# Kernel tuning notes

Hardware: AMD Instinct MI355X
Metric: run time of the kernel (lower is better)

## Reference

```python
import jax, jax.numpy as jnp
import numpy as np

B, N, DIM = 2, 2048, 1024
HEADS, DH = 16, 64
INNER = HEADS * DH
LN_EPS = 1e-5


def setup_inputs() -> dict:
    key = jax.random.key(0)
    ks = jax.random.split(key, 3)
    x = jax.random.normal(ks[0], (B, N, DIM), dtype=jnp.float32)
    ln_w = jnp.ones((DIM,), dtype=jnp.float32)
    ln_b = jnp.zeros((DIM,), dtype=jnp.float32)
    w_qkv = jax.random.normal(ks[1], (DIM, 3 * INNER), dtype=jnp.float32) * (DIM ** -0.5)
    w_out = jax.random.normal(ks[2], (INNER, DIM), dtype=jnp.float32) * (INNER ** -0.5)
    b_out = jnp.zeros((DIM,), dtype=jnp.float32)
    return {"x": x, "ln_w": ln_w, "ln_b": ln_b, "w_qkv": w_qkv, "w_out": w_out, "b_out": b_out}


def _rope(q, k):
    # q, k: (b, h, n, d) with d even; interleaved RoPE matching the torch module.
    n, d = q.shape[-2], q.shape[-1]
    inv_freq = jnp.exp(jnp.arange(0, d, 2, dtype=jnp.float32) * (-jnp.log(jnp.float32(10000.0)) / d))
    ang = jnp.arange(n, dtype=jnp.float32)[:, None] * inv_freq[None, :]  # (n, d/2)
    cos = jnp.repeat(jnp.cos(ang), 2, axis=-1)  # (n, d) -> broadcast over b,h
    sin = jnp.repeat(jnp.sin(ang), 2, axis=-1)

    def rot(t):
        t2 = t.reshape(*t.shape[:-1], d // 2, 2)  # pairs (even, odd)
        t2 = jnp.stack([-t2[..., 1], t2[..., 0]], axis=-1).reshape(t.shape)
        return t * cos + t2 * sin

    return rot(q), rot(k)


def reference(x, ln_w, ln_b, w_qkv, w_out, b_out):
    # LayerNorm
    mu = jnp.mean(x, axis=-1, keepdims=True)
    var = jnp.var(x, axis=-1, keepdims=True)
    xn = (x - mu) * jax.lax.rsqrt(var + LN_EPS) * ln_w + ln_b
    # QKV projection (no bias)
    qkv = xn @ w_qkv  # (b, n, 3*inner)
    q, k, v = jnp.split(qkv, 3, axis=-1)
    split_heads = lambda t: t.reshape(B, N, HEADS, DH).transpose(0, 2, 1, 3)  # b h n d
    q, k, v = split_heads(q), split_heads(k), split_heads(v)
    q, k = _rope(q, k)
    scale = DH ** -0.5
    dots = jnp.einsum('bhid,bhjd->bhij', q, k) * scale
    attn = jax.nn.softmax(dots, axis=-1)
    out = jnp.einsum('bhij,bhjd->bhid', attn, v)
    out = out.transpose(0, 2, 1, 3).reshape(B, N, INNER)  # b n (h d)
    return out @ w_out + b_out
```

## Files before the change

kernel.cpp:

```cpp
#include <hip/hip_runtime.h>

typedef unsigned short u16;
typedef unsigned int   u32;
typedef __bf16 bf16x8 __attribute__((ext_vector_type(8)));
typedef __bf16 bf16x2 __attribute__((ext_vector_type(2)));
typedef float  f32x4  __attribute__((ext_vector_type(4)));

#define B_     2
#define N_     2048
#define DIM_   1024
#define HEADS_ 16
#define DH_    64
#define BH_    (B_*HEADS_)
#define ROWS_  (B_*N_)

__device__ __forceinline__ u16 f2b(float f) {
  union { __bf16 h; u16 u; } v; v.h = (__bf16)f; return v.u;
}
__device__ __forceinline__ u32 pkb(float a, float b) {
  bf16x2 t; t[0] = (__bf16)a; t[1] = (__bf16)b;
  union { bf16x2 v; u32 u; } c; c.v = t; return c.u;
}
__device__ __forceinline__ float b2f(u16 h) {
  union { u32 u; float f; } v; v.u = ((u32)h) << 16;
  return v.f;
}
__device__ __forceinline__ void gload16(const void* g, void* l) {
  __builtin_amdgcn_global_load_lds(
      (const __attribute__((address_space(1))) void*)g,
      (__attribute__((address_space(3))) void*)l, 16, 0, 0);
}
__device__ __forceinline__ f32x4 mfma16(bf16x8 a, bf16x8 b, f32x4 c) {
  return __builtin_amdgcn_mfma_f32_16x16x32_bf16(a, b, c, 0, 0, 0);
}

__global__ __launch_bounds__(256) void ln_kernel(const float* __restrict__ x,
    const float* __restrict__ lw, const float* __restrict__ lb,
    u16* __restrict__ xn) {
  int r = blockIdx.x, t = threadIdx.x;
  const float4* xr = (const float4*)(x + (size_t)r * DIM_);
  float4 v = xr[t];
  float s  = v.x + v.y + v.z + v.w;
  float s2 = v.x*v.x + v.y*v.y + v.z*v.z + v.w*v.w;
  #pragma unroll
  for (int off = 32; off >= 1; off >>= 1) {
    s  += __shfl_down(s, off);
    s2 += __shfl_down(s2, off);
  }
  __shared__ float ps[4], ps2[4], bc[2];
  int w = t >> 6, lane = t & 63;
  if (lane == 0) { ps[w] = s; ps2[w] = s2; }
  __syncthreads();
  if (t == 0) {
    float S = ps[0]+ps[1]+ps[2]+ps[3], S2 = ps2[0]+ps2[1]+ps2[2]+ps2[3];
    float mu = S * (1.0f/DIM_);
    float var = S2 * (1.0f/DIM_) - mu*mu;
    bc[0] = mu; bc[1] = rsqrtf(var + 1e-5f);
  }
  __syncthreads();
  float mu = bc[0], rs = bc[1];
  float4 wv = ((const float4*)lw)[t];
  float4 bv = ((const float4*)lb)[t];
  u32 lo = pkb((v.x-mu)*rs*wv.x + bv.x, (v.y-mu)*rs*wv.y + bv.y);
  u32 hi = pkb((v.z-mu)*rs*wv.z + bv.z, (v.w-mu)*rs*wv.w + bv.w);
  ((uint2*)xn)[(size_t)r*256 + t] = make_uint2(lo, hi);
}

__global__ __launch_bounds__(256) void transpose_f32_bf16(const float* __restrict__ in,
    u16* __restrict__ out, int R, int C) {
  __shared__ float tile[32][33];
  int tx = threadIdx.x & 31, ty = threadIdx.x >> 5;
  int c0 = blockIdx.x * 32, r0 = blockIdx.y * 32;
  #pragma unroll
  for (int i = 0; i < 4; i++)
    tile[ty + i*8][tx] = in[(size_t)(r0 + ty + i*8) * C + c0 + tx];
  __syncthreads();
  #pragma unroll
  for (int i = 0; i < 4; i++)
    out[(size_t)(c0 + ty + i*8) * R + r0 + tx] = f2b(tile[tx][ty + i*8]);
}

template<int MODE>
__global__ __launch_bounds__(256) void gemm_bt(
    const u16* __restrict__ A, const u16* __restrict__ Bt, int N, int K,
    u16* __restrict__ qo, u16* __restrict__ ko, u16* __restrict__ vo,
    const float* __restrict__ bias, float* __restrict__ out) {
  __shared__ __align__(16) u16 lA[128*32];
  __shared__ __align__(16) u16 lB[128*32];
  int tid = threadIdx.x;
  int lane = tid & 63;
  int w = tid >> 6, wm = w >> 1, wn = w & 1;
  int l15 = lane & 15, g = lane >> 4;
  int bm = blockIdx.x, bn = blockIdx.y;
  const f32x4 z = {0.f, 0.f, 0.f, 0.f};
  f32x4 acc[4][4];
  #pragma unroll
  for (int i = 0; i < 4; i++)
    #pragma unroll
    for (int j = 0; j < 4; j++)
      acc[i][j] = z;
  const u16* ag = A  + (size_t)(bm*128 + (tid>>2)) * K + (tid&3)*8;
  const u16* bg = Bt + (size_t)(bn*128 + (tid>>2)) * K + (tid&3)*8;
  u16* la = lA + tid*8;
  u16* lb = lB + tid*8;
  for (int k0 = 0; k0 < K; k0 += 32) {
    gload16(ag + k0,                la);
    gload16(ag + (size_t)64*K + k0, la + 2048);
    gload16(bg + k0,                lb);
    gload16(bg + (size_t)64*K + k0, lb + 2048);
    __syncthreads();
    bf16x8 af[4], bfr[4];
    #pragma unroll
    for (int mt = 0; mt < 4; mt++)
      af[mt] = *(const bf16x8*)(lA + (wm*64 + mt*16 + l15)*32 + g*8);
    #pragma unroll
    for (int nt = 0; nt < 4; nt++)
      bfr[nt] = *(const bf16x8*)(lB + (wn*64 + nt*16 + l15)*32 + g*8);
    __builtin_amdgcn_s_setprio(1);
    #pragma unroll
    for (int mt = 0; mt < 4; mt++)
      #pragma unroll
      for (int nt = 0; nt < 4; nt++)
        acc[mt][nt] = mfma16(af[mt], bfr[nt], acc[mt][nt]);
    __builtin_amdgcn_s_setprio(0);
    __syncthreads();
  }
  #pragma unroll
  for (int mt = 0; mt < 4; mt++) {
    #pragma unroll
    for (int nt = 0; nt < 4; nt++) {
      #pragma unroll
      for (int reg = 0; reg < 4; reg++) {
        int rr = bm*128 + wm*64 + mt*16 + g*4 + reg;
        int cc = bn*128 + wn*64 + nt*16 + l15;
        float val = acc[mt][nt][reg];
        if (MODE == 0) {
          int which = cc >> 10, inner = cc & 1023;
          int h = inner >> 6, dd = inner & 63;
          int b = rr >> 11, np = rr & 2047;
          int bh = b*HEADS_ + h;
          if (which == 0)      qo[((size_t)(bh*2048 + np))*64 + dd] = f2b(val);
          else if (which == 1) ko[((size_t)(bh*2048 + np))*64 + dd] = f2b(val);
          else                 vo[((size_t)(bh*64 + dd))*2048 + np] = f2b(val);
        } else {
          out[(size_t)rr * N + cc] = val + bias[cc];
        }
      }
    }
  }
}

__global__ __launch_bounds__(256) void rope_kernel(u16* q, u16* k) {
  int tid = blockIdx.x * 256 + threadIdx.x;
  int row = tid >> 3, sub = tid & 7;
  int n = row & 2047;
  u32* qp = (u32*)(q + (size_t)row * 64 + sub * 8);
  u32* kp = (u32*)(k + (size_t)row * 64 + sub * 8);
  uint4 uq = *(uint4*)qp;
  uint4 uk = *(uint4*)kp;
  float c4[4], s4[4];
  #pragma unroll
  for (int j = 0; j < 4; j++) {
    int p = sub*4 + j;
    float freq = expf(-(2.0f * (float)p) * (9.210340371976184f / 64.0f));
    float ang = (float)n * freq;
    __sincosf(ang, &s4[j], &c4[j]);
  }
  const float qs = 0.125f * 1.4426950408889634f;
#define ROPE_Q(u, c, s) { \
    float e = b2f((u16)(u)), o = b2f((u16)((u) >> 16)); \
    (u) = pkb((e*(c) - o*(s))*qs, (o*(c) + e*(s))*qs); }
#define ROPE_K(u, c, s) { \
    float e = b2f((u16)(u)), o = b2f((u16)((u) >> 16)); \
    (u) = pkb(e*(c) - o*(s), o*(c) + e*(s)); }
  ROPE_Q(uq.x, c4[0], s4[0]) ROPE_Q(uq.y, c4[1], s4[1])
  ROPE_Q(uq.z, c4[2], s4[2]) ROPE_Q(uq.w, c4[3], s4[3])
  ROPE_K(uk.x, c4[0], s4[0]) ROPE_K(uk.y, c4[1], s4[1])
  ROPE_K(uk.z, c4[2], s4[2]) ROPE_K(uk.w, c4[3], s4[3])
#undef ROPE_Q
#undef ROPE_K
  *(uint4*)qp = uq;
  *(uint4*)kp = uk;
}

__global__ __launch_bounds__(512, 4) void flash_attn(
    const u16* __restrict__ qbf, const u16* __restrict__ kbf,
    const u16* __restrict__ vt, u16* __restrict__ aout) {
  __shared__ __align__(16) char smem[49152];
  char* lK = smem;
  char* lV = smem + 24576;
  int tid = threadIdx.x;
  int w = tid >> 6, lane = tid & 63;
  int l15 = lane & 15, g = lane >> 4;
  int p = w & 3, rho = w >> 2;
  int lin = blockIdx.x;
  int nb = (lin & 7) * 64 + (lin >> 3);
  int bh = nb >> 4, qb = nb & 15;
  const f32x4 z = {0.f, 0.f, 0.f, 0.f};
  const u16* qrow_base = qbf + ((size_t)bh*2048 + qb*128 + p*32) * 64;
  bf16x8 Qf[2][2];
  #pragma unroll
  for (int qt = 0; qt < 2; qt++)
    #pragma unroll
    for (int dh = 0; dh < 2; dh++)
      Qf[qt][dh] = *(const bf16x8*)(qrow_base + (qt*16 + l15)*64 + dh*32 + g*8);
  const char* kb = (const char*)(kbf + (size_t)bh * 2048 * 64);
  const char* vb = (const char*)(vt  + (size_t)bh * 64 * 2048);
  int srow = tid >> 3;
  int soff = ((tid & 7) * 16) ^ ((srow & 7) << 4);
  int sl = srow & 31;
  int ksrc = (srow & 32) | (((sl >> 2) & 3) << 3) | (((sl >> 4) & 1) << 2) | (sl & 3);
  const int swz = (l15 & 7) << 4;

  float lp[2][2] = {{0.f, 0.f}, {0.f, 0.f}};
  f32x4 o[4][2];
  #pragma unroll
  for (int i = 0; i < 4; i++)
    #pragma unroll
    for (int j = 0; j < 2; j++)
      o[i][j] = z;

#define STAGE(t, buf) { \
    gload16(kb + (size_t)((t)*64 + ksrc) * 128 + soff, lK + (buf)*8192 + (size_t)tid*16); \
    gload16(vb + (size_t)srow * 4096 + (t)*128 + soff, lV + (buf)*8192 + (size_t)tid*16); }

  STAGE(0, 0)
  STAGE(1, 1)
  asm volatile("s_waitcnt vmcnt(2)" ::: "memory");
  __builtin_amdgcn_s_barrier();

  int cur = 0, pfb = 2;
  #pragma unroll 1
  for (int t = 0; t < 32; ++t) {
    if (t < 30) STAGE(t + 2, pfb)
    const char* Kc = lK + cur*8192;
    const char* Vc = lV + cur*8192;
    f32x4 st[2][2];
    bf16x8 ka[2][2];
    #pragma unroll
    for (int kt = 0; kt < 2; kt++)
      #pragma unroll
      for (int dh = 0; dh < 2; dh++)
        ka[kt][dh] = *(const bf16x8*)(Kc + (rho*32 + kt*16 + l15)*128
                                         + ((dh*64 + g*16) ^ swz));
    __builtin_amdgcn_s_setprio(1);
    #pragma unroll
    for (int kt = 0; kt < 2; kt++)
      #pragma unroll
      for (int qt = 0; qt < 2; qt++) {
        f32x4 a = mfma16(ka[kt][0], Qf[qt][0], z);
        st[kt][qt] = mfma16(ka[kt][1], Qf[qt][1], a);
      }
    __builtin_amdgcn_s_setprio(0);
    #pragma unroll
    for (int kt = 0; kt < 2; kt++)
      #pragma unroll
      for (int qt = 0; qt < 2; qt++)
        #pragma unroll
        for (int r = 0; r < 4; r++) {
          float pv = __builtin_amdgcn_exp2f(st[kt][qt][r]);
          st[kt][qt][r] = pv;
          lp[qt][kt] += pv;
        }
    bf16x8 vf[4];
    #pragma unroll
    for (int dt = 0; dt < 4; dt++)
      vf[dt] = *(const bf16x8*)(Vc + (dt*16 + l15)*128 + ((rho*64 + g*16) ^ swz));
    __builtin_amdgcn_s_setprio(1);
    #pragma unroll
    for (int qt = 0; qt < 2; qt++) {
      union { u32 u[4]; bf16x8 v; } pf;
      pf.u[0] = pkb(st[0][qt][0], st[0][qt][1]);
      pf.u[1] = pkb(st[0][qt][2], st[0][qt][3]);
      pf.u[2] = pkb(st[1][qt][0], st[1][qt][1]);
      pf.u[3] = pkb(st[1][qt][2], st[1][qt][3]);
      #pragma unroll
      for (int dt = 0; dt < 4; dt++)
        o[dt][qt] = mfma16(vf[dt], pf.v, o[dt][qt]);
    }
    __builtin_amdgcn_s_setprio(0);
    if (t < 31) {
      if (t < 30) { asm volatile("s_waitcnt vmcnt(2)" ::: "memory"); }
      else        { asm volatile("s_waitcnt vmcnt(0)" ::: "memory"); }
      __builtin_amdgcn_s_barrier();
    }
    cur = (cur + 1 == 3) ? 0 : cur + 1;
    pfb = (pfb + 1 == 3) ? 0 : pfb + 1;
  }
#undef STAGE

  float ls[2];
  #pragma unroll
  for (int qt = 0; qt < 2; qt++) {
    ls[qt] = lp[qt][0] + lp[qt][1];
    ls[qt] += __shfl_xor(ls[qt], 16);
    ls[qt] += __shfl_xor(ls[qt], 32);
  }
  __syncthreads();

  float* lspx = (float*)(smem + 32768);
  if (rho == 1) {
    #pragma unroll
    for (int dt = 0; dt < 4; dt++)
      #pragma unroll
      for (int qt = 0; qt < 2; qt++) {
        int ql = qt*16 + l15;
        int off = p*8192 + ql*256 + ((dt*64 + g*16) ^ ((ql & 7) << 4));
        *(f32x4*)(smem + off) = o[dt][qt];
      }
    if (g == 0) {
      lspx[p*64 + l15]      = ls[0];
      lspx[p*64 + 16 + l15] = ls[1];
    }
  }
  __syncthreads();
  float rls[2] = {0.f, 0.f};
  if (rho == 0) {
    #pragma unroll
    for (int qt = 0; qt < 2; qt++)
      rls[qt] = 1.0f / (ls[qt] + lspx[p*64 + qt*16 + l15]);
    #pragma unroll
    for (int dt = 0; dt < 4; dt++)
      #pragma unroll
      for (int qt = 0; qt < 2; qt++) {
        int ql = qt*16 + l15;
        int off = p*8192 + ql*256 + ((dt*64 + g*16) ^ ((ql & 7) << 4));
        o[dt][qt] += *(const f32x4*)(smem + off);
      }
  }
  __syncthreads();
  if (rho == 0) {
    #pragma unroll
    for (int dt = 0; dt < 4; dt++)
      #pragma unroll
      for (int qt = 0; qt < 2; qt++) {
        int ql = qt*16 + l15;
        u32 w0 = pkb(o[dt][qt][0]*rls[qt], o[dt][qt][1]*rls[qt]);
        u32 w1 = pkb(o[dt][qt][2]*rls[qt], o[dt][qt][3]*rls[qt]);
        int d2 = dt*32 + g*8;
        *(uint2*)(smem + p*8192 + ql*128 + (d2 ^ ((ql & 7) << 4))) =
            make_uint2(w0, w1);
      }
  }
  __syncthreads();
  int row = tid >> 2;
  int b = bh >> 4, h = bh & 15;
  int n = qb*128 + row;
  #pragma unroll
  for (int j = 0; j < 2; j++) {
    int slot = (tid & 3)*2 + j;
    uint4 rv = *(const uint4*)(smem + (row >> 5)*8192 + (row & 31)*128
                               + ((slot*16) ^ ((row & 7) << 4)));
    *(uint4*)(aout + ((size_t)(b*2048 + n))*1024 + h*64 + slot*8) = rv;
  }
}

extern "C" void kernel_launch(void* const* d_in, const int* in_sizes, int n_in,
                              void* d_out, int out_size, void* d_ws, size_t ws_size,
                              hipStream_t stream) {
  const float* x    = (const float*)d_in[0];
  const float* lw   = (const float*)d_in[1];
  const float* lb   = (const float*)d_in[2];
  const float* wqkv = (const float*)d_in[3];
  const float* wout = (const float*)d_in[4];
  const float* bout = (const float*)d_in[5];
  float* out = (float*)d_out;

  char* ws = (char*)d_ws;
  size_t off = 0;
  auto alloc = [&](size_t bytes) {
    char* p = ws + off;
    off += (bytes + 255) & ~(size_t)255;
    return p;
  };
  u16* xn   = (u16*)alloc((size_t)ROWS_*DIM_*2);
  u16* wqt  = (u16*)alloc((size_t)3072*1024*2);
  u16* wot  = (u16*)alloc((size_t)1024*1024*2);
  u16* qb   = (u16*)alloc((size_t)BH_*2048*64*2);
  u16* kb   = (u16*)alloc((size_t)BH_*2048*64*2);
  u16* vtb  = (u16*)alloc((size_t)BH_*2048*64*2);
  u16* aout = (u16*)alloc((size_t)ROWS_*1024*2);

  ln_kernel<<<ROWS_, 256, 0, stream>>>(x, lw, lb, xn);
  transpose_f32_bf16<<<dim3(96, 32), 256, 0, stream>>>(wqkv, wqt, 1024, 3072);
  transpose_f32_bf16<<<dim3(32, 32), 256, 0, stream>>>(wout, wot, 1024, 1024);
  gemm_bt<0><<<dim3(32, 24), 256, 0, stream>>>(xn, wqt, 3072, 1024,
                                               qb, kb, vtb, nullptr, nullptr);
  rope_kernel<<<2048, 256, 0, stream>>>(qb, kb);
  flash_attn<<<512, 512, 0, stream>>>(qb, kb, vtb, aout);
  gemm_bt<1><<<dim3(32, 8), 256, 0, stream>>>(aout, wot, 1024, 1024,
                                              nullptr, nullptr, nullptr, bout, out);
}
```

Measured before the change: 124.5 us.

## Replace QKV GEMM with 256x256-tile double-buffered kernel using swizzled LDS

Adds a dedicated QKV projection GEMM with 256x256 output tiles, 512 threads, BK=64, double-buffered direct global-to-LDS loads with an XOR swizzle, and interleaved LDS reads and MFMA issue under raised wave priority. Blocks are remapped so that consecutive blocks share B tiles, for better L2 reuse. The larger tile is meant to raise arithmetic intensity and overlap loads with compute. The costs are 128KB of LDS per block, heavy register pressure from a 32-tile accumulator, and only 192 blocks on a 256-CU device, which leaves some CUs idle.

```diff
diff --git a/kernel.cpp b/kernel.cpp
--- a/kernel.cpp
+++ b/kernel.cpp
@@ -78,6 +78,102 @@
   #pragma unroll
   for (int i = 0; i < 4; i++)
     out[(size_t)(c0 + ty + i*8) * R + r0 + tx] = f2b(tile[tx][ty + i*8]);
+}
+
+__global__ __launch_bounds__(512, 2) void gemm256_qkv(
+    const u16* __restrict__ A, const u16* __restrict__ Bt,
+    u16* __restrict__ qo, u16* __restrict__ ko, u16* __restrict__ vo) {
+  __shared__ __align__(16) char lds[131072];
+  const int K = 1024;
+  int tid = threadIdx.x;
+  int lane = tid & 63;
+  int w = tid >> 6, wm = w >> 2, wn = w & 3;
+  int l15 = lane & 15, g = lane >> 4;
+  int lin = blockIdx.x;
+  int nb = (lin & 7) * 24 + (lin >> 3);
+  int bm = nb & 15, bn = nb >> 4;
+  int srow = tid >> 3;
+  int ssoff = ((tid & 7) * 16) ^ ((srow & 7) << 4);
+  const char* Ab = (const char*)A;
+  const char* Bb = (const char*)Bt;
+  const int swz = (l15 & 7) << 4;
+
+  f32x4 acc[8][4];
+  #pragma unroll
+  for (int i = 0; i < 8; i++)
+    #pragma unroll
+    for (int j = 0; j < 4; j++)
+      acc[i][j] = (f32x4){0.f, 0.f, 0.f, 0.f};
+
+#define SA(t, buf) { _Pragma("unroll") for (int j = 0; j < 4; j++) \
+    gload16(Ab + ((size_t)(bm*256 + j*64 + srow) * K + (size_t)(t)*64) * 2 + ssoff, \
+            lds + (buf)*65536 + j*8192 + tid*16); }
+#define SB(t, buf) { _Pragma("unroll") for (int j = 0; j < 4; j++) \
+    gload16(Bb + ((size_t)(bn*256 + j*64 + srow) * K + (size_t)(t)*64) * 2 + ssoff, \
+            lds + (buf)*65536 + 32768 + j*8192 + tid*16); }
+#define RDA(qm) { _Pragma("unroll") for (int mt = 0; mt < 4; mt++) { \
+    const char* ar = lA + (wm*128 + ((qm)*4 + mt)*16 + l15)*128; \
+    af[mt][0] = *(const bf16x8*)(ar + ((g*16) ^ swz)); \
+    af[mt][1] = *(const bf16x8*)(ar + ((64 + g*16) ^ swz)); } }
+#define RDB(qn) { _Pragma("unroll") for (int nt = 0; nt < 2; nt++) { \
+    const char* br = lB + (wn*64 + ((qn)*2 + nt)*16 + l15)*128; \
+    bfr[nt][0] = *(const bf16x8*)(br + ((g*16) ^ swz)); \
+    bfr[nt][1] = *(const bf16x8*)(br + ((64 + g*16) ^ swz)); } }
+#define MM(qm, qn) { __builtin_amdgcn_s_setprio(1); \
+    _Pragma("unroll") for (int mt = 0; mt < 4; mt++) \
+    _Pragma("unroll") for (int nt = 0; nt < 2; nt++) { \
+      f32x4 c = acc[(qm)*4 + mt][(qn)*2 + nt]; \
+      c = mfma16(af[mt][0], bfr[nt][0], c); \
+      c = mfma16(af[mt][1], bfr[nt][1], c); \
+      acc[(qm)*4 + mt][(qn)*2 + nt] = c; } \
+    __builtin_amdgcn_s_setprio(0); }
+
+  SA(0, 0) SB(0, 0) SA(1, 1) SB(1, 1)
+  __syncthreads();
+
+  #pragma unroll 1
+  for (int t = 0; t < 16; ++t) {
+    const char* lA = lds + (t & 1)*65536;
+    const char* lB = lA + 32768;
+    int nbuf = (t + 1) & 1;
+    bf16x8 af[4][2], bfr[2][2];
+    RDA(0) RDB(0)
+    if (t >= 1 && t < 15) SA(t + 1, nbuf)
+    MM(0, 0)
+    RDB(1)
+    if (t >= 1 && t < 15) SB(t + 1, nbuf)
+    MM(0, 1)
+    RDA(1) RDB(0)
+    MM(1, 0)
+    RDB(1)
+    MM(1, 1)
+    if (t < 15) __syncthreads();
+  }
+#undef SA
+#undef SB
+#undef RDA
+#undef RDB
+#undef MM
+
+  #pragma unroll
+  for (int mi = 0; mi < 8; mi++) {
+    #pragma unroll
+    for (int ni = 0; ni < 4; ni++) {
+      #pragma unroll
+      for (int reg = 0; reg < 4; reg++) {
+        int rr = bm*256 + wm*128 + mi*16 + g*4 + reg;
+        int cc = bn*256 + wn*64 + ni*16 + l15;
+        float val = acc[mi][ni][reg];
+        int which = cc >> 10, inner = cc & 1023;
+        int h = inner >> 6, dd = inner & 63;
+        int b = rr >> 11, np = rr & 2047;
+        int bh = b*HEADS_ + h;
+        if (which == 0)      qo[((size_t)(bh*2048 + np))*64 + dd] = f2b(val);
+        else if (which == 1) ko[((size_t)(bh*2048 + np))*64 + dd] = f2b(val);
+        else                 vo[((size_t)(bh*64 + dd))*2048 + np] = f2b(val);
+      }
+    }
+  }
 }
 
 template<int MODE>
@@ -384,8 +480,7 @@
   ln_kernel<<<ROWS_, 256, 0, stream>>>(x, lw, lb, xn);
   transpose_f32_bf16<<<dim3(96, 32), 256, 0, stream>>>(wqkv, wqt, 1024, 3072);
   transpose_f32_bf16<<<dim3(32, 32), 256, 0, stream>>>(wout, wot, 1024, 1024);
-  gemm_bt<0><<<dim3(32, 24), 256, 0, stream>>>(xn, wqt, 3072, 1024,
-                                               qb, kb, vtb, nullptr, nullptr);
+  gemm256_qkv<<<192, 512, 0, stream>>>(xn, wqt, qb, kb, vtb);
   rope_kernel<<<2048, 256, 0, stream>>>(qb, kb);
   flash_attn<<<512, 512, 0, stream>>>(qb, kb, vtb, aout);
   gemm_bt<1><<<dim3(32, 8), 256, 0, stream>>>(aout, wot, 1024, 1024,
```

Result: slower. 140.1 us (+12.5%).

## Fuse prep kernels, fold RoPE into QKV GEMM epilogue, retile output GEMM

Applied to the files above, without the earlier changes.

Merges layernorm, both weight transposes and a cos/sin table build into one prep launch. RoPE and the query scale are applied inside the QKV GEMM epilogue, with the partner element fetched by lane shuffle, which removes the separate RoPE read/write pass over Q and K. The output projection GEMM becomes a dedicated kernel with 128x64 tiles, doubling the block count for better CU occupancy. The trade-offs are extra cos/sin table loads per epilogue element and more total B-tile traffic in the output GEMM.

```diff
diff --git a/kernel.cpp b/kernel.cpp
--- a/kernel.cpp
+++ b/kernel.cpp
@@ -34,57 +34,76 @@
   return __builtin_amdgcn_mfma_f32_16x16x32_bf16(a, b, c, 0, 0, 0);
 }
 
-__global__ __launch_bounds__(256) void ln_kernel(const float* __restrict__ x,
-    const float* __restrict__ lw, const float* __restrict__ lb,
-    u16* __restrict__ xn) {
-  int r = blockIdx.x, t = threadIdx.x;
-  const float4* xr = (const float4*)(x + (size_t)r * DIM_);
-  float4 v = xr[t];
-  float s  = v.x + v.y + v.z + v.w;
-  float s2 = v.x*v.x + v.y*v.y + v.z*v.z + v.w*v.w;
-  #pragma unroll
-  for (int off = 32; off >= 1; off >>= 1) {
-    s  += __shfl_down(s, off);
-    s2 += __shfl_down(s2, off);
-  }
-  __shared__ float ps[4], ps2[4], bc[2];
-  int w = t >> 6, lane = t & 63;
-  if (lane == 0) { ps[w] = s; ps2[w] = s2; }
-  __syncthreads();
-  if (t == 0) {
-    float S = ps[0]+ps[1]+ps[2]+ps[3], S2 = ps2[0]+ps2[1]+ps2[2]+ps2[3];
-    float mu = S * (1.0f/DIM_);
-    float var = S2 * (1.0f/DIM_) - mu*mu;
-    bc[0] = mu; bc[1] = rsqrtf(var + 1e-5f);
-  }
-  __syncthreads();
-  float mu = bc[0], rs = bc[1];
-  float4 wv = ((const float4*)lw)[t];
-  float4 bv = ((const float4*)lb)[t];
-  u32 lo = pkb((v.x-mu)*rs*wv.x + bv.x, (v.y-mu)*rs*wv.y + bv.y);
-  u32 hi = pkb((v.z-mu)*rs*wv.z + bv.z, (v.w-mu)*rs*wv.w + bv.w);
-  ((uint2*)xn)[(size_t)r*256 + t] = make_uint2(lo, hi);
-}
-
-__global__ __launch_bounds__(256) void transpose_f32_bf16(const float* __restrict__ in,
-    u16* __restrict__ out, int R, int C) {
+__global__ __launch_bounds__(256) void prep_kernel(
+    const float* __restrict__ x, const float* __restrict__ lw,
+    const float* __restrict__ lb, const float* __restrict__ wqkv,
+    const float* __restrict__ wout, u16* __restrict__ xn,
+    u16* __restrict__ wqt, u16* __restrict__ wot,
+    float* __restrict__ cosT, float* __restrict__ sinT) {
   __shared__ float tile[32][33];
-  int tx = threadIdx.x & 31, ty = threadIdx.x >> 5;
-  int c0 = blockIdx.x * 32, r0 = blockIdx.y * 32;
-  #pragma unroll
-  for (int i = 0; i < 4; i++)
-    tile[ty + i*8][tx] = in[(size_t)(r0 + ty + i*8) * C + c0 + tx];
-  __syncthreads();
-  #pragma unroll
-  for (int i = 0; i < 4; i++)
-    out[(size_t)(c0 + ty + i*8) * R + r0 + tx] = f2b(tile[tx][ty + i*8]);
-}
-
-template<int MODE>
-__global__ __launch_bounds__(256) void gemm_bt(
-    const u16* __restrict__ A, const u16* __restrict__ Bt, int N, int K,
-    u16* __restrict__ qo, u16* __restrict__ ko, u16* __restrict__ vo,
-    const float* __restrict__ bias, float* __restrict__ out) {
+  int blk = blockIdx.x, t = threadIdx.x;
+  if (blk < 4096) {
+    int r = blk;
+    const float4* xr = (const float4*)(x + (size_t)r * DIM_);
+    float4 v = xr[t];
+    float s  = v.x + v.y + v.z + v.w;
+    float s2 = v.x*v.x + v.y*v.y + v.z*v.z + v.w*v.w;
+    #pragma unroll
+    for (int off = 32; off >= 1; off >>= 1) {
+      s  += __shfl_down(s, off);
+      s2 += __shfl_down(s2, off);
+    }
+    int w = t >> 6, lane = t & 63;
+    if (lane == 0) { tile[0][w] = s; tile[1][w] = s2; }
+    __syncthreads();
+    if (t == 0) {
+      float S = tile[0][0]+tile[0][1]+tile[0][2]+tile[0][3];
+      float S2 = tile[1][0]+tile[1][1]+tile[1][2]+tile[1][3];
+      float mu = S * (1.0f/DIM_);
+      float var = S2 * (1.0f/DIM_) - mu*mu;
+      tile[2][0] = mu; tile[2][1] = rsqrtf(var + 1e-5f);
+    }
+    __syncthreads();
+    float mu = tile[2][0], rs = tile[2][1];
+    float4 wv = ((const float4*)lw)[t];
+    float4 bv = ((const float4*)lb)[t];
+    u32 lo = pkb((v.x-mu)*rs*wv.x + bv.x, (v.y-mu)*rs*wv.y + bv.y);
+    u32 hi = pkb((v.z-mu)*rs*wv.z + bv.z, (v.w-mu)*rs*wv.w + bv.w);
+    ((uint2*)xn)[(size_t)r*256 + t] = make_uint2(lo, hi);
+  } else if (blk < 8192) {
+    const float* in; u16* outp; int R, C, c0, r0;
+    if (blk < 7168) {
+      int b2 = blk - 4096;
+      in = wqkv; outp = wqt; R = 1024; C = 3072;
+      c0 = (b2 % 96) * 32; r0 = (b2 / 96) * 32;
+    } else {
+      int b2 = blk - 7168;
+      in = wout; outp = wot; R = 1024; C = 1024;
+      c0 = (b2 & 31) * 32; r0 = (b2 >> 5) * 32;
+    }
+    int tx = t & 31, ty = t >> 5;
+    #pragma unroll
+    for (int i = 0; i < 4; i++)
+      tile[ty + i*8][tx] = in[(size_t)(r0 + ty + i*8) * C + c0 + tx];
+    __syncthreads();
+    #pragma unroll
+    for (int i = 0; i < 4; i++)
+      outp[(size_t)(c0 + ty + i*8) * R + r0 + tx] = f2b(tile[tx][ty + i*8]);
+  } else {
+    int tid = (blk - 8192) * 256 + t;
+    int n = tid >> 5, p = tid & 31;
+    float freq = expf(-(2.0f * (float)p) * (9.210340371976184f / 64.0f));
+    float ang = (float)n * freq;
+    cosT[tid] = cosf(ang);
+    sinT[tid] = sinf(ang);
+  }
+}
+
+__global__ __launch_bounds__(256) void gemm_qkv(
+    const u16* __restrict__ A, const u16* __restrict__ Bt,
+    const float* __restrict__ cosT, const float* __restrict__ sinT,
+    u16* __restrict__ qo, u16* __restrict__ ko, u16* __restrict__ vo) {
+  const int K = 1024;
   __shared__ __align__(16) u16 lA[128*32];
   __shared__ __align__(16) u16 lB[128*32];
   int tid = threadIdx.x;
@@ -125,6 +144,7 @@
     __builtin_amdgcn_s_setprio(0);
     __syncthreads();
   }
+  const float qs = 0.125f * 1.4426950408889634f;
   #pragma unroll
   for (int mt = 0; mt < 4; mt++) {
     #pragma unroll
@@ -134,53 +154,80 @@
         int rr = bm*128 + wm*64 + mt*16 + g*4 + reg;
         int cc = bn*128 + wn*64 + nt*16 + l15;
         float val = acc[mt][nt][reg];
-        if (MODE == 0) {
-          int which = cc >> 10, inner = cc & 1023;
-          int h = inner >> 6, dd = inner & 63;
-          int b = rr >> 11, np = rr & 2047;
-          int bh = b*HEADS_ + h;
-          if (which == 0)      qo[((size_t)(bh*2048 + np))*64 + dd] = f2b(val);
-          else if (which == 1) ko[((size_t)(bh*2048 + np))*64 + dd] = f2b(val);
-          else                 vo[((size_t)(bh*64 + dd))*2048 + np] = f2b(val);
-        } else {
-          out[(size_t)rr * N + cc] = val + bias[cc];
+        int which = cc >> 10, inner = cc & 1023;
+        int h = inner >> 6, dd = inner & 63;
+        int b = rr >> 11, np = rr & 2047;
+        int bh = b*HEADS_ + h;
+        if (which < 2) {
+          float pv = __shfl_xor(val, 1);
+          int p = dd >> 1;
+          float c = cosT[np*32 + p];
+          float s = sinT[np*32 + p];
+          val = (dd & 1) ? (val*c + pv*s) : (val*c - pv*s);
+          if (which == 0) val *= qs;
         }
-      }
-    }
-  }
-}
-
-__global__ __launch_bounds__(256) void rope_kernel(u16* q, u16* k) {
-  int tid = blockIdx.x * 256 + threadIdx.x;
-  int row = tid >> 3, sub = tid & 7;
-  int n = row & 2047;
-  u32* qp = (u32*)(q + (size_t)row * 64 + sub * 8);
-  u32* kp = (u32*)(k + (size_t)row * 64 + sub * 8);
-  uint4 uq = *(uint4*)qp;
-  uint4 uk = *(uint4*)kp;
-  float c4[4], s4[4];
-  #pragma unroll
-  for (int j = 0; j < 4; j++) {
-    int p = sub*4 + j;
-    float freq = expf(-(2.0f * (float)p) * (9.210340371976184f / 64.0f));
-    float ang = (float)n * freq;
-    __sincosf(ang, &s4[j], &c4[j]);
-  }
-  const float qs = 0.125f * 1.4426950408889634f;
-#define ROPE_Q(u, c, s) { \
-    float e = b2f((u16)(u)), o = b2f((u16)((u) >> 16)); \
-    (u) = pkb((e*(c) - o*(s))*qs, (o*(c) + e*(s))*qs); }
-#define ROPE_K(u, c, s) { \
-    float e = b2f((u16)(u)), o = b2f((u16)((u) >> 16)); \
-    (u) = pkb(e*(c) - o*(s), o*(c) + e*(s)); }
-  ROPE_Q(uq.x, c4[0], s4[0]) ROPE_Q(uq.y, c4[1], s4[1])
-  ROPE_Q(uq.z, c4[2], s4[2]) ROPE_Q(uq.w, c4[3], s4[3])
-  ROPE_K(uk.x, c4[0], s4[0]) ROPE_K(uk.y, c4[1], s4[1])
-  ROPE_K(uk.z, c4[2], s4[2]) ROPE_K(uk.w, c4[3], s4[3])
-#undef ROPE_Q
-#undef ROPE_K
-  *(uint4*)qp = uq;
-  *(uint4*)kp = uk;
+        if (which == 0)      qo[((size_t)(bh*2048 + np))*64 + dd] = f2b(val);
+        else if (which == 1) ko[((size_t)(bh*2048 + np))*64 + dd] = f2b(val);
+        else                 vo[((size_t)(bh*64 + dd))*2048 + np] = f2b(val);
+      }
+    }
+  }
+}
+
+__global__ __launch_bounds__(256) void gemm_out(
+    const u16* __restrict__ A, const u16* __restrict__ Bt,
+    const float* __restrict__ bias, float* __restrict__ out) {
+  const int K = 1024, N = 1024;
+  __shared__ __align__(16) u16 lA[128*32];
+  __shared__ __align__(16) u16 lB[64*32];
+  int tid = threadIdx.x;
+  int lane = tid & 63;
+  int w = tid >> 6, wm = w >> 1, wn = w & 1;
+  int l15 = lane & 15, g = lane >> 4;
+  int bm = blockIdx.x, bn = blockIdx.y;
+  const f32x4 z = {0.f, 0.f, 0.f, 0.f};
+  f32x4 acc[4][2];
+  #pragma unroll
+  for (int i = 0; i < 4; i++)
+    #pragma unroll
+    for (int j = 0; j < 2; j++)
+      acc[i][j] = z;
+  const u16* ag = A  + (size_t)(bm*128 + (tid>>2)) * K + (tid&3)*8;
+  const u16* bg = Bt + (size_t)(bn*64 + (tid>>2)) * K + (tid&2)*8;
+  bg = Bt + (size_t)(bn*64 + (tid>>2)) * K + (tid&3)*8;
+  u16* la = lA + tid*8;
+  u16* lb = lB + tid*8;
+  for (int k0 = 0; k0 < K; k0 += 32) {
+    gload16(ag + k0,                la);
+    gload16(ag + (size_t)64*K + k0, la + 2048);
+    if (tid < 256) gload16(bg + k0, lb);
+    __syncthreads();
+    bf16x8 af[4], bfr[2];
+    #pragma unroll
+    for (int mt = 0; mt < 4; mt++)
+      af[mt] = *(const bf16x8*)(lA + (wm*64 + mt*16 + l15)*32 + g*8);
+    #pragma unroll
+    for (int nt = 0; nt < 2; nt++)
+      bfr[nt] = *(const bf16x8*)(lB + (wn*32 + nt*16 + l15)*32 + g*8);
+    __builtin_amdgcn_s_setprio(1);
+    #pragma unroll
+    for (int mt = 0; mt < 4; mt++)
+      #pragma unroll
+      for (int nt = 0; nt < 2; nt++)
+        acc[mt][nt] = mfma16(af[mt], bfr[nt], acc[mt][nt]);
+    __builtin_amdgcn_s_setprio(0);
+    __syncthreads();
+  }
+  #pragma unroll
+  for (int mt = 0; mt < 4; mt++)
+    #pragma unroll
+    for (int nt = 0; nt < 2; nt++)
+      #pragma unroll
+      for (int reg = 0; reg < 4; reg++) {
+        int rr = bm*128 + wm*64 + mt*16 + g*4 + reg;
+        int cc = bn*64 + wn*32 + nt*16 + l15;
+        out[(size_t)rr * N + cc] = acc[mt][nt][reg] + bias[cc];
+      }
 }
 
 __global__ __launch_bounds__(512, 4) void flash_attn(
@@ -380,14 +427,13 @@
   u16* kb   = (u16*)alloc((size_t)BH_*2048*64*2);
   u16* vtb  = (u16*)alloc((size_t)BH_*2048*64*2);
   u16* aout = (u16*)alloc((size_t)ROWS_*1024*2);
-
-  ln_kernel<<<ROWS_, 256, 0, stream>>>(x, lw, lb, xn);
-  transpose_f32_bf16<<<dim3(96, 32), 256, 0, stream>>>(wqkv, wqt, 1024, 3072);
-  transpose_f32_bf16<<<dim3(32, 32), 256, 0, stream>>>(wout, wot, 1024, 1024);
-  gemm_bt<0><<<dim3(32, 24), 256, 0, stream>>>(xn, wqt, 3072, 1024,
-                                               qb, kb, vtb, nullptr, nullptr);
-  rope_kernel<<<2048, 256, 0, stream>>>(qb, kb);
+  float* cosT = (float*)alloc((size_t)2048*32*4);
+  float* sinT = (float*)alloc((size_t)2048*32*4);
+
+  prep_kernel<<<8448, 256, 0, stream>>>(x, lw, lb, wqkv, wout,
+                                        xn, wqt, wot, cosT, sinT);
+  gemm_qkv<<<dim3(32, 24), 256, 0, stream>>>(xn, wqt, cosT, sinT,
+                                             qb, kb, vtb);
   flash_attn<<<512, 512, 0, stream>>>(qb, kb, vtb, aout);
-  gemm_bt<1><<<dim3(32, 8), 256, 0, stream>>>(aout, wot, 1024, 1024,
-                                              nullptr, nullptr, nullptr, bout, out);
-}
+  gemm_out<<<dim3(32, 16), 256, 0, stream>>>(aout, wot, bout, out);
+}
```

New measurement: 138.2 us. +11.0%, slower.
